# Performance work log

Hardware: AMD Instinct MI355X
Metric: run time of the kernel (lower is better)

The kernel has to match this reference:

```python
import jax, jax.numpy as jnp
import numpy as np

PACK = 8  # 32-bit words / 4-bit weights
GROUP = 128


def _unpack4(q):
    # q: [E, K//8, N] int32 packed nibbles -> [E, K, N] ints in [0, 15]
    nib = jnp.stack([(q >> (4 * j)) & 0xF for j in range(PACK)], axis=2)
    E, Kp, _, N = nib.shape
    return nib.reshape(E, Kp * PACK, N)


def _dequant(qweight, scales, g_idx):
    # GPTQ symmetric 4-bit: w = (nibble - 8) * scale[group(k), n]
    # g_idx (desc_act) maps each input row k to its quantization group,
    # equivalent math to Marlin's sorted-g_idx activation reordering.
    w = _unpack4(qweight).astype(jnp.float32) - 8.0          # [E, K, N]
    s = jnp.take_along_axis(scales, g_idx[:, :, None].astype(jnp.int32), axis=1)
    return w * s


def reference(x, router_logits, w13_qweight, w2_qweight,
              w13_scales, w2_scales, w13_g_idx, w2_g_idx, top_k):
    T = x.shape[0]
    E = w13_qweight.shape[0]
    W13 = _dequant(w13_qweight, w13_scales, w13_g_idx)   # [E, H, 2I]
    W2 = _dequant(w2_qweight, w2_scales, w2_g_idx)       # [E, I, H]
    I = W2.shape[1]

    # routing: softmax -> top-k -> renormalize
    probs = jax.nn.softmax(router_logits, axis=-1)       # [T, E]
    tw, tid = jax.lax.top_k(probs, top_k)                # [T, k]
    tw = tw / jnp.sum(tw, axis=-1, keepdims=True)
    cw = jnp.zeros((T, E), x.dtype).at[jnp.arange(T)[:, None], tid].add(tw)

    # grouped GEMM over all experts, weighted combine
    h = jnp.einsum('th,ehn->etn', x, W13)                # [E, T, 2I]
    gate, up = h[..., :I], h[..., I:]
    act = jax.nn.silu(gate) * up                         # [E, T, I]
    out_e = jnp.einsum('eti,eih->eth', act, W2)          # [E, T, H]
    return jnp.einsum('eth,te->th', out_e, cw)           # [T, H]


def setup_inputs() -> dict:
    key = jax.random.key(0)
    ks = jax.random.split(key, 8)
    T, E, H, I = 2048, 8, 1024, 4096
    x = jax.random.normal(ks[0], (T, H), dtype=jnp.float32)
    router_logits = jax.random.normal(ks[1], (T, E), dtype=jnp.float32)
    w13_qweight = jax.random.randint(ks[2], (E, H // PACK, 2 * I), 0, 2147483647, dtype=jnp.int32)
    w2_qweight = jax.random.randint(ks[3], (E, I // PACK, H), 0, 2147483647, dtype=jnp.int32)
    w13_scales = jax.random.uniform(ks[4], (E, H // GROUP, 2 * I), dtype=jnp.float32) * 0.02
    w2_scales = jax.random.uniform(ks[5], (E, I // GROUP, H), dtype=jnp.float32) * 0.02
    w13_g_idx = jax.random.randint(ks[6], (E, H), 0, H // GROUP, dtype=jnp.int32)
    w2_g_idx = jax.random.randint(ks[7], (E, I), 0, I // GROUP, dtype=jnp.int32)
    return {
        'x': x, 'router_logits': router_logits,
        'w13_qweight': w13_qweight, 'w2_qweight': w2_qweight,
        'w13_scales': w13_scales, 'w2_scales': w2_scales,
        'w13_g_idx': w13_g_idx, 'w2_g_idx': w2_g_idx,
        'top_k': 2,
    }
```

## Files before the change

### kernel.cpp

```cpp
#include <hip/hip_runtime.h>

#define T_TOK 2048
#define NEXP  8
#define H_DIM 1024
#define I_DIM 4096

#define N13  (2*I_DIM)
#define N2   (H_DIM)
#define NG13 8
#define NG2  32

#define KSPLIT2 4
#define KLEN2 (I_DIM/KSPLIT2)
#define BK   64

#define MAXT2 40

typedef __bf16 bf16x8 __attribute__((ext_vector_type(8)));
typedef float  f32x4  __attribute__((ext_vector_type(4)));

#define GLD_LDS(g, l) \
  __builtin_amdgcn_global_load_lds((const __attribute__((address_space(1))) void*)(g), \
                                   (__attribute__((address_space(3))) void*)(l), 16, 0, 0)

#define WS_OFFS   64
#define WS_PLIST  (WS_OFFS  + 64)
#define WS_PW     (WS_PLIST + 2*T_TOK*4)
#define WS_WL     65792
#define WS_NTS    66176
#define WS_SPOS   66432
#define PAIR_PAD  (2*T_TOK + 128)
#define WS_XG     131072
#define WS_ACT    (WS_XG  + PAIR_PAD*H_DIM*2)
#define WS_B1T    (WS_ACT + (size_t)PAIR_PAD*I_DIM*2)
#define WS_W2T    (WS_B1T + (size_t)NEXP*N13*H_DIM*2)

__global__ __launch_bounds__(512) void k_route(
    const float* __restrict__ logits,
    int* __restrict__ offs,
    int* __restrict__ plist, float* __restrict__ pw,
    int* __restrict__ spos,
    int* __restrict__ wl, int* __restrict__ nts) {

    __shared__ int cnt[NEXP], cur[NEXP];
    __shared__ short se[2*T_TOK];
    __shared__ float swt[2*T_TOK];

    const int tid = threadIdx.x;
    if (tid < NEXP) cnt[tid] = 0;
    __syncthreads();

    for (int t = tid; t < T_TOK; t += 512) {
        float l[NEXP];
        #pragma unroll
        for (int e = 0; e < NEXP; e++) l[e] = logits[t * NEXP + e];
        int i0 = 0; float b0 = l[0];
        #pragma unroll
        for (int e = 1; e < NEXP; e++) if (l[e] > b0) { b0 = l[e]; i0 = e; }
        int i1 = -1; float b1 = -1e30f;
        #pragma unroll
        for (int e = 0; e < NEXP; e++) if (e != i0 && l[e] > b1) { b1 = l[e]; i1 = e; }
        float w1 = 1.f / (1.f + __expf(b0 - b1));
        float w0 = 1.f - w1;
        se[2*t] = (short)i0; se[2*t+1] = (short)i1;
        swt[2*t] = w0; swt[2*t+1] = w1;
        atomicAdd(&cnt[i0], 1);
        atomicAdd(&cnt[i1], 1);
    }
    __syncthreads();

    if (tid == 0) {
        int s = 0;
        for (int e = 0; e < NEXP; e++) { offs[e] = s; cur[e] = s; s += cnt[e]; }
        offs[NEXP] = s;
        int n = 0;
        for (int e = 0; e < NEXP; e++)
            for (int mt = 0; mt * 128 < cnt[e]; mt++) wl[n++] = (e << 8) | mt;
        nts[0] = n;
    }
    __syncthreads();

    for (int t = tid; t < T_TOK; t += 512) {
        #pragma unroll
        for (int s = 0; s < 2; s++) {
            int e = se[2*t+s];
            int pos = atomicAdd(&cur[e], 1);
            plist[pos] = t;
            pw[pos] = swt[2*t+s];
            spos[2*t+s] = pos;
        }
    }
}

__global__ void k_gather(const float* __restrict__ x, const int* __restrict__ plist,
                         __bf16* __restrict__ xg) {
    int p = blockIdx.x;
    int t = plist[p];
    int i = threadIdx.x;
    const f32x4* src = reinterpret_cast<const f32x4*>(x + (size_t)t * H_DIM);
    f32x4 v0 = src[i*2], v1 = src[i*2+1];
    __align__(16) __bf16 tb[8];
    #pragma unroll
    for (int j = 0; j < 4; j++) { tb[j] = (__bf16)v0[j]; tb[4+j] = (__bf16)v1[j]; }
    *reinterpret_cast<f32x4*>(xg + (size_t)p * H_DIM + i*8) = *reinterpret_cast<f32x4*>(tb);
}

template<bool INTERLEAVE>
__global__ __launch_bounds__(256) void k_dequant(
    const int* __restrict__ q, const float* __restrict__ s, const int* __restrict__ g,
    __bf16* __restrict__ outw, int R, int K, int N, int NG) {

    const int e  = blockIdx.z;
    const int r0 = blockIdx.x * 64;
    const int k0 = blockIdx.y * 128;
    const int*   qe = q + (size_t)e * (K/8) * N;
    const float* se = s + (size_t)e * NG * N;
    const int*   ge = g + (size_t)e * K + k0;
    __bf16*      oe = outw + (size_t)e * R * K;

    __shared__ __align__(16) __bf16 tile[64][128];

    const int t  = threadIdx.x;
    const int rl = t & 63, kq = t >> 6;
    const int r  = r0 + rl;
    const int S  = INTERLEAVE ? (((r >> 4) << 3) + (r & 7) + (((r >> 3) & 1) ? (N >> 1) : 0))
                              : r;
    #pragma unroll
    for (int jj = 0; jj < 4; jj++) {
        int kp = kq + jj*4;
        int qv = qe[(size_t)(k0/8 + kp) * N + S];
        __align__(16) __bf16 tmp[8];
        #pragma unroll
        for (int j2 = 0; j2 < 8; j2++) {
            float sc = se[(size_t)ge[kp*8 + j2] * N + S];
            tmp[j2] = (__bf16)((float)(((qv >> (4*j2)) & 15) - 8) * sc);
        }
        int c = kp ^ (rl & 15);
        *reinterpret_cast<f32x4*>(&tile[rl][c*8]) = *reinterpret_cast<f32x4*>(tmp);
    }
    __syncthreads();
    #pragma unroll
    for (int i = 0; i < 4; i++) {
        int sidx = t + i*256;
        int row = sidx >> 4, ch = sidx & 15;
        int cs = ch ^ (row & 15);
        *reinterpret_cast<f32x4*>(oe + (size_t)(r0+row)*K + k0 + ch*8)
            = *reinterpret_cast<const f32x4*>(&tile[row][cs*8]);
    }
}

#define VM3 asm volatile("s_waitcnt vmcnt(3)" ::: "memory")
#define VM0 asm volatile("s_waitcnt vmcnt(0)" ::: "memory")
#define LGK0 { asm volatile("s_waitcnt lgkmcnt(0)" ::: "memory"); __builtin_amdgcn_sched_barrier(0); }
#define BARRIER  { __builtin_amdgcn_s_barrier(); __builtin_amdgcn_sched_barrier(0); }
#define SCHEDFENCE __builtin_amdgcn_sched_barrier(0)

__global__ __launch_bounds__(512) void k_gemm1(
    const __bf16* __restrict__ xg,
    const __bf16* __restrict__ B1t,
    const int*    __restrict__ offs,
    const float*  __restrict__ pw,
    const int*    __restrict__ wl,
    const int*    __restrict__ nts,
    __bf16*       __restrict__ act) {

    const int ti = blockIdx.x >> 5;
    if (ti >= nts[0]) return;
    const int nb = blockIdx.x & 31;
    const int w  = wl[ti];
    const int e  = w >> 8, mt = w & 255;
    const int m0 = offs[e] + mt * 128;
    const int mcount = min(offs[e+1] - m0, 128);
    const int n0r = nb * 256;

    __shared__ __align__(16) __bf16 AsF[2*2*4096];
    __shared__ __align__(16) __bf16 BsF[2*2*8192];
    __shared__ float wts[128];

    const int tid = threadIdx.x;
    const int wv = tid >> 6, lane = tid & 63;
    const int lrow = lane & 15, quad = lane >> 4;
    const int wr = (wv >> 2) * 64;
    const int wc = (wv & 3) * 64;
    const int cq = quad ^ ((lrow >> 1) & 3);

    for (int m = tid; m < 128; m += 512)
        wts[m] = (m < mcount) ? pw[m0 + m] : 0.f;

    const __bf16* Abase = xg  + (size_t)m0 * H_DIM;
    const __bf16* Bbase = B1t + ((size_t)e * N13 + n0r) * H_DIM;

    f32x4 acc[4][4];
    #pragma unroll
    for (int i = 0; i < 4; i++)
        #pragma unroll
        for (int j = 0; j < 4; j++) acc[i][j] = (f32x4)(0.f);

    auto stageA = [&](int prt, int h2, int kt) {
        const __bf16* g = Abase + kt * BK + h2 * 32;
        __bf16* d = AsF + prt * 8192 + h2 * 4096;
        int row = tid >> 2;
        int gch = (tid & 3) ^ ((row >> 1) & 3);
        int rowc = min(row, mcount - 1);
        GLD_LDS(g + (size_t)rowc * H_DIM + gch * 8, d + tid * 8);
    };
    auto stageB = [&](int prt, int h2, int kt) {
        const __bf16* g = Bbase + kt * BK + h2 * 32;
        __bf16* d = BsF + prt * 16384 + h2 * 8192;
        #pragma unroll
        for (int q2 = 0; q2 < 2; q2++) {
            int row = (tid >> 2) + q2 * 128;
            int gch = (tid & 3) ^ ((row >> 1) & 3);
            GLD_LDS(g + (size_t)row * H_DIM + gch * 8, d + tid * 8 + q2 * 4096);
        }
    };

    stageA(0, 0, 0); stageB(0, 0, 0); stageA(0, 1, 0); stageB(0, 1, 0);

    const int NT = H_DIM / BK;
    for (int kt = 0; kt < NT; kt++) {
        const int prt = kt & 1, nxt = prt ^ 1;
        const bool st = (kt + 1 < NT);
        const __bf16* Ab = AsF + prt * 8192;
        const __bf16* Bb = BsF + prt * 16384;
        #pragma unroll
        for (int h2 = 0; h2 < 2; h2++) {
            if (h2 == 0) { VM3; } else if (st) { VM3; } else { VM0; }
            BARRIER;
            {
                bf16x8 bb[4], a[4];
                #pragma unroll
                for (int j = 0; j < 4; j++)
                    bb[j] = *reinterpret_cast<const bf16x8*>(
                        &Bb[h2*8192 + (wc + 16*j + lrow)*32 + cq*8]);
                #pragma unroll
                for (int i = 0; i < 4; i++)
                    a[i] = *reinterpret_cast<const bf16x8*>(
                        &Ab[h2*4096 + (wr + 16*i + lrow)*32 + cq*8]);
                if (st) { stageA(nxt, h2, kt + 1); stageB(nxt, h2, kt + 1); }
                LGK0;
                __builtin_amdgcn_s_setprio(1);
                #pragma unroll
                for (int j = 0; j < 4; j++)
                    #pragma unroll
                    for (int i = 0; i < 4; i++)
                        acc[i][j] = __builtin_amdgcn_mfma_f32_16x16x32_bf16(a[i], bb[j], acc[i][j], 0, 0, 0);
                __builtin_amdgcn_s_setprio(0);
            }
            SCHEDFENCE;
        }
    }

    #pragma unroll
    for (int j = 0; j < 4; j++) {
        const int c0 = ((n0r + wc + 16*j) >> 1);
        #pragma unroll
        for (int i = 0; i < 4; i++)
            #pragma unroll
            for (int rr = 0; rr < 4; rr++) {
                float v = acc[i][j][rr];
                float partner = __shfl_xor(v, 8, 64);
                int m = wr + 16*i + quad*4 + rr;
                if (lrow < 8 && m < mcount) {
                    float gg = v, uu = partner;
                    float a = (gg / (1.f + __expf(-gg))) * uu * wts[m];
                    act[(size_t)(m0 + m) * I_DIM + c0 + lrow] = (__bf16)a;
                }
            }
    }
}

__global__ __launch_bounds__(512) void k_gemm2(
    const __bf16* __restrict__ act,
    const __bf16* __restrict__ W2t,
    const int*    __restrict__ offs,
    const int*    __restrict__ wl,
    const int*    __restrict__ nts,
    float*        __restrict__ outp) {

    const int ti = blockIdx.x >> 4;
    if (ti >= nts[0]) return;
    const int nb = (blockIdx.x >> 2) & 3;
    const int ks = blockIdx.x & 3;
    const int w  = wl[ti];
    const int e  = w >> 8, mt = w & 255;
    const int m0 = offs[e] + mt * 128;
    const int mcount = min(offs[e+1] - m0, 128);
    const int n0 = nb * 256;
    const int kz = ks * KLEN2;

    __shared__ __align__(16) __bf16 AsF[2*2*4096];
    __shared__ __align__(16) __bf16 BsF[2*2*8192];

    const int tid = threadIdx.x;
    const int wv = tid >> 6, lane = tid & 63;
    const int lrow = lane & 15, quad = lane >> 4;
    const int wr = (wv >> 2) * 64;
    const int wc = (wv & 3) * 64;
    const int cq = quad ^ ((lrow >> 1) & 3);

    const __bf16* Abase = act + (size_t)m0 * I_DIM + kz;
    const __bf16* Bbase = W2t + ((size_t)e * N2 + n0) * I_DIM + kz;

    f32x4 acc[4][4];
    #pragma unroll
    for (int i = 0; i < 4; i++)
        #pragma unroll
        for (int j = 0; j < 4; j++) acc[i][j] = (f32x4)(0.f);

    auto stageA = [&](int prt, int h2, int kt) {
        const __bf16* g = Abase + kt * BK + h2 * 32;
        __bf16* d = AsF + prt * 8192 + h2 * 4096;
        int row = tid >> 2;
        int gch = (tid & 3) ^ ((row >> 1) & 3);
        int rowc = min(row, mcount - 1);
        GLD_LDS(g + (size_t)rowc * I_DIM + gch * 8, d + tid * 8);
    };
    auto stageB = [&](int prt, int h2, int kt) {
        const __bf16* g = Bbase + kt * BK + h2 * 32;
        __bf16* d = BsF + prt * 16384 + h2 * 8192;
        #pragma unroll
        for (int q2 = 0; q2 < 2; q2++) {
            int row = (tid >> 2) + q2 * 128;
            int gch = (tid & 3) ^ ((row >> 1) & 3);
            GLD_LDS(g + (size_t)row * I_DIM + gch * 8, d + tid * 8 + q2 * 4096);
        }
    };

    stageA(0, 0, 0); stageB(0, 0, 0); stageA(0, 1, 0); stageB(0, 1, 0);

    const int NT = KLEN2 / BK;
    for (int kt = 0; kt < NT; kt++) {
        const int prt = kt & 1, nxt = prt ^ 1;
        const bool st = (kt + 1 < NT);
        const __bf16* Ab = AsF + prt * 8192;
        const __bf16* Bb = BsF + prt * 16384;
        #pragma unroll
        for (int h2 = 0; h2 < 2; h2++) {
            if (h2 == 0) { VM3; } else if (st) { VM3; } else { VM0; }
            BARRIER;
            {
                bf16x8 bb[4], a[4];
                #pragma unroll
                for (int j = 0; j < 4; j++)
                    bb[j] = *reinterpret_cast<const bf16x8*>(
                        &Bb[h2*8192 + (wc + 16*j + lrow)*32 + cq*8]);
                #pragma unroll
                for (int i = 0; i < 4; i++)
                    a[i] = *reinterpret_cast<const bf16x8*>(
                        &Ab[h2*4096 + (wr + 16*i + lrow)*32 + cq*8]);
                if (st) { stageA(nxt, h2, kt + 1); stageB(nxt, h2, kt + 1); }
                LGK0;
                __builtin_amdgcn_s_setprio(1);
                #pragma unroll
                for (int j = 0; j < 4; j++)
                    #pragma unroll
                    for (int i = 0; i < 4; i++)
                        acc[i][j] = __builtin_amdgcn_mfma_f32_16x16x32_bf16(a[i], bb[j], acc[i][j], 0, 0, 0);
                __builtin_amdgcn_s_setprio(0);
            }
            SCHEDFENCE;
        }
    }

    float* op = outp + ((size_t)ks * PAIR_PAD + m0) * N2;
    #pragma unroll
    for (int j = 0; j < 4; j++) {
        int h = n0 + wc + 16*j + lrow;
        #pragma unroll
        for (int i = 0; i < 4; i++)
            #pragma unroll
            for (int rr = 0; rr < 4; rr++) {
                int m = wr + 16*i + quad*4 + rr;
                if (m < mcount)
                    op[(size_t)m * N2 + h] = acc[i][j][rr];
            }
    }
}

__global__ __launch_bounds__(256) void k_reduce(
    const float* __restrict__ outp, const int* __restrict__ spos,
    float* __restrict__ out) {
    const int t  = blockIdx.x;
    const int h4 = threadIdx.x;
    const int p0 = spos[2*t], p1 = spos[2*t+1];
    const f32x4* r0 = reinterpret_cast<const f32x4*>(outp + (size_t)p0 * H_DIM) + h4;
    const f32x4* r1 = reinterpret_cast<const f32x4*>(outp + (size_t)p1 * H_DIM) + h4;
    f32x4 acc = (f32x4)(0.f);
    #pragma unroll
    for (int ks = 0; ks < KSPLIT2; ks++) {
        size_t off = (size_t)ks * (PAIR_PAD * (H_DIM/4));
        acc += r0[off] + r1[off];
    }
    reinterpret_cast<f32x4*>(out + (size_t)t * H_DIM)[h4] = acc;
}

extern "C" void kernel_launch(void* const* d_in, const int* in_sizes, int n_in,
                              void* d_out, int out_size, void* d_ws, size_t ws_size,
                              hipStream_t stream) {
    const float* x      = (const float*)d_in[0];
    const float* logits = (const float*)d_in[1];
    const int*   w13q   = (const int*)  d_in[2];
    const int*   w2q    = (const int*)  d_in[3];
    const float* w13s   = (const float*)d_in[4];
    const float* w2s    = (const float*)d_in[5];
    const int*   g13    = (const int*)  d_in[6];
    const int*   g2     = (const int*)  d_in[7];

    char* ws = (char*)d_ws;
    int*    offs   = (int*)   (ws + WS_OFFS);
    int*    plist  = (int*)   (ws + WS_PLIST);
    float*  pw     = (float*) (ws + WS_PW);
    int*    wl     = (int*)   (ws + WS_WL);
    int*    nts    = (int*)   (ws + WS_NTS);
    int*    spos   = (int*)   (ws + WS_SPOS);
    __bf16* xg     = (__bf16*)(ws + WS_XG);
    __bf16* act    = (__bf16*)(ws + WS_ACT);
    __bf16* B1t    = (__bf16*)(ws + WS_B1T);
    __bf16* W2t    = (__bf16*)(ws + WS_W2T);
    float*  outp   = (float*) (ws + WS_B1T);
    float*  out    = (float*) d_out;

    k_dequant<true ><<<dim3(N13/64, H_DIM/128, NEXP), 256, 0, stream>>>(
        w13q, w13s, g13, B1t, N13, H_DIM, N13, NG13);
    k_dequant<false><<<dim3(N2/64,  I_DIM/128, NEXP), 256, 0, stream>>>(
        w2q,  w2s,  g2,  W2t, N2,  I_DIM, N2,  NG2);

    k_route <<<1, 512, 0, stream>>>(logits, offs, plist, pw, spos, wl, nts);
    k_gather<<<2*T_TOK, 128, 0, stream>>>(x, plist, xg);

    k_gemm1<<<MAXT2 * 32, 512, 0, stream>>>(xg, B1t, offs, pw, wl, nts, act);
    k_gemm2<<<MAXT2 * 16, 512, 0, stream>>>(act, W2t, offs, wl, nts, outp);
    k_reduce<<<T_TOK, 256, 0, stream>>>(outp, spos, out);
}
```

Measured before the change: 362.5 us.

## Enlarge expert GEMM M-tile to 256 rows with split A/B staging phases

Both grouped GEMM kernels now process 256 tokens per tile instead of 128. Each wave computes a 128x64 output block (8x4 MFMA accumulators) with the B fragments reused across two A half-blocks. The routing worklist is rebuilt with 256-row tiles, and the launch grids shrink to match. The aim is to halve the number of times the dequantized expert weights are streamed from memory per expert. In exchange it doubles accumulator registers and A-tile LDS, adds an extra barrier per half-step, and leaves fewer, larger blocks with more padding waste on partial tiles.

```diff
diff --git a/kernel.cpp b/kernel.cpp
--- a/kernel.cpp
+++ b/kernel.cpp
@@ -14,7 +14,7 @@
 #define KLEN2 (I_DIM/KSPLIT2)
 #define BK   64
 
-#define MAXT2 40
+#define MAXT1 24
 
 typedef __bf16 bf16x8 __attribute__((ext_vector_type(8)));
 typedef float  f32x4  __attribute__((ext_vector_type(4)));
@@ -75,7 +75,7 @@
         offs[NEXP] = s;
         int n = 0;
         for (int e = 0; e < NEXP; e++)
-            for (int mt = 0; mt * 128 < cnt[e]; mt++) wl[n++] = (e << 8) | mt;
+            for (int mt = 0; mt * 256 < cnt[e]; mt++) wl[n++] = (e << 8) | mt;
         nts[0] = n;
     }
     __syncthreads();
@@ -149,7 +149,7 @@
     }
 }
 
-#define VM3 asm volatile("s_waitcnt vmcnt(3)" ::: "memory")
+#define VM4 asm volatile("s_waitcnt vmcnt(4)" ::: "memory")
 #define VM0 asm volatile("s_waitcnt vmcnt(0)" ::: "memory")
 #define LGK0 { asm volatile("s_waitcnt lgkmcnt(0)" ::: "memory"); __builtin_amdgcn_sched_barrier(0); }
 #define BARRIER  { __builtin_amdgcn_s_barrier(); __builtin_amdgcn_sched_barrier(0); }
@@ -169,40 +169,43 @@
     const int nb = blockIdx.x & 31;
     const int w  = wl[ti];
     const int e  = w >> 8, mt = w & 255;
-    const int m0 = offs[e] + mt * 128;
-    const int mcount = min(offs[e+1] - m0, 128);
+    const int m0 = offs[e] + mt * 256;
+    const int mcount = min(offs[e+1] - m0, 256);
     const int n0r = nb * 256;
 
-    __shared__ __align__(16) __bf16 AsF[2*2*4096];
+    __shared__ __align__(16) __bf16 AsF[2*2*8192];
     __shared__ __align__(16) __bf16 BsF[2*2*8192];
-    __shared__ float wts[128];
+    __shared__ float wts[256];
 
     const int tid = threadIdx.x;
     const int wv = tid >> 6, lane = tid & 63;
     const int lrow = lane & 15, quad = lane >> 4;
-    const int wr = (wv >> 2) * 64;
+    const int wr = (wv >> 2) * 128;
     const int wc = (wv & 3) * 64;
     const int cq = quad ^ ((lrow >> 1) & 3);
 
-    for (int m = tid; m < 128; m += 512)
+    for (int m = tid; m < 256; m += 512)
         wts[m] = (m < mcount) ? pw[m0 + m] : 0.f;
 
     const __bf16* Abase = xg  + (size_t)m0 * H_DIM;
     const __bf16* Bbase = B1t + ((size_t)e * N13 + n0r) * H_DIM;
 
-    f32x4 acc[4][4];
-    #pragma unroll
-    for (int i = 0; i < 4; i++)
+    f32x4 acc[8][4];
+    #pragma unroll
+    for (int i = 0; i < 8; i++)
         #pragma unroll
         for (int j = 0; j < 4; j++) acc[i][j] = (f32x4)(0.f);
 
     auto stageA = [&](int prt, int h2, int kt) {
         const __bf16* g = Abase + kt * BK + h2 * 32;
-        __bf16* d = AsF + prt * 8192 + h2 * 4096;
-        int row = tid >> 2;
-        int gch = (tid & 3) ^ ((row >> 1) & 3);
-        int rowc = min(row, mcount - 1);
-        GLD_LDS(g + (size_t)rowc * H_DIM + gch * 8, d + tid * 8);
+        __bf16* d = AsF + prt * 16384 + h2 * 8192;
+        #pragma unroll
+        for (int q2 = 0; q2 < 2; q2++) {
+            int row = (tid >> 2) + q2 * 128;
+            int gch = (tid & 3) ^ ((row >> 1) & 3);
+            int rowc = min(row, mcount - 1);
+            GLD_LDS(g + (size_t)rowc * H_DIM + gch * 8, d + tid * 8 + q2 * 4096);
+        }
     };
     auto stageB = [&](int prt, int h2, int kt) {
         const __bf16* g = Bbase + kt * BK + h2 * 32;
@@ -221,23 +224,24 @@
     for (int kt = 0; kt < NT; kt++) {
         const int prt = kt & 1, nxt = prt ^ 1;
         const bool st = (kt + 1 < NT);
-        const __bf16* Ab = AsF + prt * 8192;
+        const __bf16* Ab = AsF + prt * 16384;
         const __bf16* Bb = BsF + prt * 16384;
         #pragma unroll
         for (int h2 = 0; h2 < 2; h2++) {
-            if (h2 == 0) { VM3; } else if (st) { VM3; } else { VM0; }
+            bf16x8 bb[4];
+            if (h2 == 0) { VM4; } else if (st) { VM4; } else { VM0; }
             BARRIER;
             {
-                bf16x8 bb[4], a[4];
                 #pragma unroll
                 for (int j = 0; j < 4; j++)
                     bb[j] = *reinterpret_cast<const bf16x8*>(
                         &Bb[h2*8192 + (wc + 16*j + lrow)*32 + cq*8]);
+                bf16x8 a[4];
                 #pragma unroll
                 for (int i = 0; i < 4; i++)
                     a[i] = *reinterpret_cast<const bf16x8*>(
-                        &Ab[h2*4096 + (wr + 16*i + lrow)*32 + cq*8]);
-                if (st) { stageA(nxt, h2, kt + 1); stageB(nxt, h2, kt + 1); }
+                        &Ab[h2*8192 + (wr + 16*i + lrow)*32 + cq*8]);
+                if (st) stageA(nxt, h2, kt + 1);
                 LGK0;
                 __builtin_amdgcn_s_setprio(1);
                 #pragma unroll
@@ -248,6 +252,24 @@
                 __builtin_amdgcn_s_setprio(0);
             }
             SCHEDFENCE;
+            BARRIER;
+            {
+                bf16x8 a[4];
+                #pragma unroll
+                for (int i = 0; i < 4; i++)
+                    a[i] = *reinterpret_cast<const bf16x8*>(
+                        &Ab[h2*8192 + (wr + 64 + 16*i + lrow)*32 + cq*8]);
+                if (st) stageB(nxt, h2, kt + 1);
+                LGK0;
+                __builtin_amdgcn_s_setprio(1);
+                #pragma unroll
+                for (int j = 0; j < 4; j++)
+                    #pragma unroll
+                    for (int i = 0; i < 4; i++)
+                        acc[4+i][j] = __builtin_amdgcn_mfma_f32_16x16x32_bf16(a[i], bb[j], acc[4+i][j], 0, 0, 0);
+                __builtin_amdgcn_s_setprio(0);
+            }
+            SCHEDFENCE;
         }
     }
 
@@ -255,7 +277,7 @@
     for (int j = 0; j < 4; j++) {
         const int c0 = ((n0r + wc + 16*j) >> 1);
         #pragma unroll
-        for (int i = 0; i < 4; i++)
+        for (int i = 0; i < 8; i++)
             #pragma unroll
             for (int rr = 0; rr < 4; rr++) {
                 float v = acc[i][j][rr];
@@ -284,37 +306,40 @@
     const int ks = blockIdx.x & 3;
     const int w  = wl[ti];
     const int e  = w >> 8, mt = w & 255;
-    const int m0 = offs[e] + mt * 128;
-    const int mcount = min(offs[e+1] - m0, 128);
+    const int m0 = offs[e] + mt * 256;
+    const int mcount = min(offs[e+1] - m0, 256);
     const int n0 = nb * 256;
     const int kz = ks * KLEN2;
 
-    __shared__ __align__(16) __bf16 AsF[2*2*4096];
+    __shared__ __align__(16) __bf16 AsF[2*2*8192];
     __shared__ __align__(16) __bf16 BsF[2*2*8192];
 
     const int tid = threadIdx.x;
     const int wv = tid >> 6, lane = tid & 63;
     const int lrow = lane & 15, quad = lane >> 4;
-    const int wr = (wv >> 2) * 64;
+    const int wr = (wv >> 2) * 128;
     const int wc = (wv & 3) * 64;
     const int cq = quad ^ ((lrow >> 1) & 3);
 
     const __bf16* Abase = act + (size_t)m0 * I_DIM + kz;
     const __bf16* Bbase = W2t + ((size_t)e * N2 + n0) * I_DIM + kz;
 
-    f32x4 acc[4][4];
-    #pragma unroll
-    for (int i = 0; i < 4; i++)
+    f32x4 acc[8][4];
+    #pragma unroll
+    for (int i = 0; i < 8; i++)
         #pragma unroll
         for (int j = 0; j < 4; j++) acc[i][j] = (f32x4)(0.f);
 
     auto stageA = [&](int prt, int h2, int kt) {
         const __bf16* g = Abase + kt * BK + h2 * 32;
-        __bf16* d = AsF + prt * 8192 + h2 * 4096;
-        int row = tid >> 2;
-        int gch = (tid & 3) ^ ((row >> 1) & 3);
-        int rowc = min(row, mcount - 1);
-        GLD_LDS(g + (size_t)rowc * I_DIM + gch * 8, d + tid * 8);
+        __bf16* d = AsF + prt * 16384 + h2 * 8192;
+        #pragma unroll
+        for (int q2 = 0; q2 < 2; q2++) {
+            int row = (tid >> 2) + q2 * 128;
+            int gch = (tid & 3) ^ ((row >> 1) & 3);
+            int rowc = min(row, mcount - 1);
+            GLD_LDS(g + (size_t)rowc * I_DIM + gch * 8, d + tid * 8 + q2 * 4096);
+        }
     };
     auto stageB = [&](int prt, int h2, int kt) {
         const __bf16* g = Bbase + kt * BK + h2 * 32;
@@ -333,23 +358,24 @@
     for (int kt = 0; kt < NT; kt++) {
         const int prt = kt & 1, nxt = prt ^ 1;
         const bool st = (kt + 1 < NT);
-        const __bf16* Ab = AsF + prt * 8192;
+        const __bf16* Ab = AsF + prt * 16384;
         const __bf16* Bb = BsF + prt * 16384;
         #pragma unroll
         for (int h2 = 0; h2 < 2; h2++) {
-            if (h2 == 0) { VM3; } else if (st) { VM3; } else { VM0; }
+            bf16x8 bb[4];
+            if (h2 == 0) { VM4; } else if (st) { VM4; } else { VM0; }
             BARRIER;
             {
-                bf16x8 bb[4], a[4];
                 #pragma unroll
                 for (int j = 0; j < 4; j++)
                     bb[j] = *reinterpret_cast<const bf16x8*>(
                         &Bb[h2*8192 + (wc + 16*j + lrow)*32 + cq*8]);
+                bf16x8 a[4];
                 #pragma unroll
                 for (int i = 0; i < 4; i++)
                     a[i] = *reinterpret_cast<const bf16x8*>(
-                        &Ab[h2*4096 + (wr + 16*i + lrow)*32 + cq*8]);
-                if (st) { stageA(nxt, h2, kt + 1); stageB(nxt, h2, kt + 1); }
+                        &Ab[h2*8192 + (wr + 16*i + lrow)*32 + cq*8]);
+                if (st) stageA(nxt, h2, kt + 1);
                 LGK0;
                 __builtin_amdgcn_s_setprio(1);
                 #pragma unroll
@@ -360,6 +386,24 @@
                 __builtin_amdgcn_s_setprio(0);
             }
             SCHEDFENCE;
+            BARRIER;
+            {
+                bf16x8 a[4];
+                #pragma unroll
+                for (int i = 0; i < 4; i++)
+                    a[i] = *reinterpret_cast<const bf16x8*>(
+                        &Ab[h2*8192 + (wr + 64 + 16*i + lrow)*32 + cq*8]);
+                if (st) stageB(nxt, h2, kt + 1);
+                LGK0;
+                __builtin_amdgcn_s_setprio(1);
+                #pragma unroll
+                for (int j = 0; j < 4; j++)
+                    #pragma unroll
+                    for (int i = 0; i < 4; i++)
+                        acc[4+i][j] = __builtin_amdgcn_mfma_f32_16x16x32_bf16(a[i], bb[j], acc[4+i][j], 0, 0, 0);
+                __builtin_amdgcn_s_setprio(0);
+            }
+            SCHEDFENCE;
         }
     }
 
@@ -368,7 +412,7 @@
     for (int j = 0; j < 4; j++) {
         int h = n0 + wc + 16*j + lrow;
         #pragma unroll
-        for (int i = 0; i < 4; i++)
+        for (int i = 0; i < 8; i++)
             #pragma unroll
             for (int rr = 0; rr < 4; rr++) {
                 int m = wr + 16*i + quad*4 + rr;
@@ -429,7 +473,7 @@
     k_route <<<1, 512, 0, stream>>>(logits, offs, plist, pw, spos, wl, nts);
     k_gather<<<2*T_TOK, 128, 0, stream>>>(x, plist, xg);
 
-    k_gemm1<<<MAXT2 * 32, 512, 0, stream>>>(xg, B1t, offs, pw, wl, nts, act);
-    k_gemm2<<<MAXT2 * 16, 512, 0, stream>>>(act, W2t, offs, wl, nts, outp);
+    k_gemm1<<<MAXT1 * 32, 512, 0, stream>>>(xg, B1t, offs, pw, wl, nts, act);
+    k_gemm2<<<MAXT1 * 16, 512, 0, stream>>>(act, W2t, offs, wl, nts, outp);
     k_reduce<<<T_TOK, 256, 0, stream>>>(outp, spos, out);
 }
```

Result: slower. 389.1 us (+7.3%).
